# Optimization experiments

Measured on AMD Instinct MI355X. Metric: run time of the kernel, lower is better.

Reference implementation:

```python
import jax, jax.numpy as jnp
import numpy as np

N = 100000      # nodes
E = 1000000     # edges
G = 1024        # graphs
NODE_IN, CLIMBER_IN, HID, OUT, HEADS = 6, 4, 64, 4, 2
SLOPE = 0.2     # PyG GATConv default negative_slope


def gat_conv(x, edge_index, W, att_src, att_dst, bias):
    """PyG GATConv, heads=HEADS, concat=False (mean over heads), add_self_loops=True."""
    heads, ch = att_src.shape
    xp = (x @ W).reshape(-1, heads, ch)                       # [N,H,C]
    a_src = jnp.einsum('nhc,hc->nh', xp, att_src)             # [N,H]
    a_dst = jnp.einsum('nhc,hc->nh', xp, att_dst)
    loops = jnp.arange(x.shape[0])
    src = jnp.concatenate([edge_index[0], loops])             # [E+N]
    dst = jnp.concatenate([edge_index[1], loops])
    e = jax.nn.leaky_relu(a_src[src] + a_dst[dst], SLOPE)     # [E+N,H]
    emax = jax.ops.segment_max(e, dst, num_segments=x.shape[0])
    emax = jnp.where(jnp.isfinite(emax), emax, 0.0)
    ex = jnp.exp(e - emax[dst])
    den = jax.ops.segment_sum(ex, dst, num_segments=x.shape[0])
    alpha = ex / (den[dst] + 1e-16)                           # segment softmax over incoming edges
    msg = xp[src] * alpha[:, :, None]                         # [E+N,H,C]
    agg = jax.ops.segment_sum(msg, dst, num_segments=x.shape[0])  # [N,H,C]
    return agg.mean(axis=1) + bias                            # concat=False -> head mean


def setup_inputs() -> dict:
    key = jax.random.key(0)
    ks = jax.random.split(key, 20)
    s = lambda *d: 1.0 / np.sqrt(d[0])
    inp = {
        'x': jax.random.normal(ks[0], (N, NODE_IN), jnp.float32),
        'edge_index': jax.random.randint(ks[1], (2, E), 0, N),
        'batch': jnp.sort(jax.random.randint(ks[2], (N,), 0, G)),
        'climber': jax.random.normal(ks[3], (G, CLIMBER_IN), jnp.float32),
        # conv1 params
        'W1': jax.random.normal(ks[4], (NODE_IN, HEADS * HID), jnp.float32) * s(NODE_IN),
        'as1': jax.random.normal(ks[5], (HEADS, HID), jnp.float32) * s(HID),
        'ad1': jax.random.normal(ks[6], (HEADS, HID), jnp.float32) * s(HID),
        'b1': jnp.zeros((HID,), jnp.float32),
        # conv2 params
        'W2': jax.random.normal(ks[7], (HID, HEADS * HID), jnp.float32) * s(HID),
        'as2': jax.random.normal(ks[8], (HEADS, HID), jnp.float32) * s(HID),
        'ad2': jax.random.normal(ks[9], (HEADS, HID), jnp.float32) * s(HID),
        'b2': jnp.zeros((HID,), jnp.float32),
        # climber embed
        'Wc': jax.random.normal(ks[10], (CLIMBER_IN, HID), jnp.float32) * s(CLIMBER_IN),
        'bc': jnp.zeros((HID,), jnp.float32),
        # classifier
        'Wm1': jax.random.normal(ks[11], (2 * HID, HID), jnp.float32) * s(2 * HID),
        'bm1': jnp.zeros((HID,), jnp.float32),
        'Wm2': jax.random.normal(ks[12], (HID, OUT), jnp.float32) * s(HID),
        'bm2': jnp.zeros((OUT,), jnp.float32),
    }
    return inp


def reference(x, edge_index, batch, climber, W1, as1, ad1, b1, W2, as2, ad2, b2,
              Wc, bc, Wm1, bm1, Wm2, bm2):
    h = jax.nn.relu(gat_conv(x, edge_index, W1, as1, ad1, b1))
    h = jax.nn.relu(gat_conv(h, edge_index, W2, as2, ad2, b2))
    c = jax.nn.relu(climber @ Wc + bc)            # dropout is identity in eval mode
    z = jnp.concatenate([h, c[batch]], axis=1)    # [N, 2*HID]
    z = jax.nn.relu(z @ Wm1 + bm1)                # dropout identity (eval)
    return z @ Wm2 + bm2                          # [N, OUT]
```

## Files before the change

### kernel.cpp

```cpp
#include <hip/hip_runtime.h>
#include <hip/hip_fp16.h>

#define SLOPE 0.2f
#define BKW  512
#define BKSH 9
#define MAXB 256

typedef _Float16 half8 __attribute__((ext_vector_type(8)));
typedef float f32x4 __attribute__((ext_vector_type(4)));

__device__ __forceinline__ float lrelu(float v) { return v >= 0.f ? v : SLOPE * v; }

__device__ __forceinline__ unsigned pack2(float a, float b) {
    __half2 h = __floats2half2_rn(a, b);
    return *reinterpret_cast<unsigned*>(&h);
}
__device__ __forceinline__ float2 h2f(unsigned u) {
    __half2 h = *reinterpret_cast<__half2*>(&u);
    return __half22float2(h);
}

__device__ __forceinline__ void pk8(unsigned& A0, unsigned& A1, unsigned& A2, unsigned& A3,
                                    unsigned ap, uint4 u) {
    __half2 a = *reinterpret_cast<__half2*>(&ap);
    __half2* up = reinterpret_cast<__half2*>(&u);
    *reinterpret_cast<__half2*>(&A0) = __hfma2(up[0], a, *reinterpret_cast<__half2*>(&A0));
    *reinterpret_cast<__half2*>(&A1) = __hfma2(up[1], a, *reinterpret_cast<__half2*>(&A1));
    *reinterpret_cast<__half2*>(&A2) = __hfma2(up[2], a, *reinterpret_cast<__half2*>(&A2));
    *reinterpret_cast<__half2*>(&A3) = __hfma2(up[3], a, *reinterpret_cast<__half2*>(&A3));
}

__global__ __launch_bounds__(256)
void k_xp_gemm64h(const __half* __restrict__ x, const _Float16* __restrict__ W2t,
                  const float* __restrict__ as_, const float* __restrict__ ad_,
                  __half* __restrict__ xph, float* __restrict__ asrc,
                  float* __restrict__ adst, int N) {
    __shared__ __half lh[4][16][128];
    const int t = threadIdx.x;
    const int w = t >> 6, lane = t & 63;
    const int c8 = lane & 15, kgrp = lane >> 4;
    const int nr0 = blockIdx.x * 64 + w * 16;

    uint4 a0u = make_uint4(0u,0u,0u,0u), a1u = make_uint4(0u,0u,0u,0u);
    int ar = nr0 + c8;
    if (ar < N) {
        const uint4* hp = (const uint4*)(x + (size_t)ar * 64);
        a0u = hp[kgrp];
        a1u = hp[4 + kgrp];
    }
    half8 A0, A1;
    __builtin_memcpy(&A0, &a0u, 16);
    __builtin_memcpy(&A1, &a1u, 16);

    f32x4 acc[8];
    #pragma unroll
    for (int i = 0; i < 8; ++i) acc[i] = (f32x4){0.f, 0.f, 0.f, 0.f};

    #pragma unroll
    for (int ct = 0; ct < 8; ++ct) {
        const uint4* wp = (const uint4*)(W2t + (size_t)(ct * 16 + c8) * 64);
        uint4 b0u = wp[kgrp];
        uint4 b1u = wp[4 + kgrp];
        half8 B0, B1;
        __builtin_memcpy(&B0, &b0u, 16);
        __builtin_memcpy(&B1, &b1u, 16);
        acc[ct] = __builtin_amdgcn_mfma_f32_16x16x32_f16(A0, B0, acc[ct], 0, 0, 0);
        acc[ct] = __builtin_amdgcn_mfma_f32_16x16x32_f16(A1, B1, acc[ct], 0, 0, 0);
    }

    float ps0[4] = {0,0,0,0}, ps1[4] = {0,0,0,0};
    float pd0[4] = {0,0,0,0}, pd1[4] = {0,0,0,0};
    #pragma unroll
    for (int ct = 0; ct < 8; ++ct) {
        float av = as_[ct * 16 + c8];
        float dv = ad_[ct * 16 + c8];
        #pragma unroll
        for (int j = 0; j < 4; ++j) {
            float v = acc[ct][j];
            if (ct < 4) { ps0[j] += av * v; pd0[j] += dv * v; }
            else        { ps1[j] += av * v; pd1[j] += dv * v; }
        }
    }
    #pragma unroll
    for (int off = 1; off <= 8; off <<= 1) {
        #pragma unroll
        for (int j = 0; j < 4; ++j) {
            ps0[j] += __shfl_xor(ps0[j], off, 64);
            ps1[j] += __shfl_xor(ps1[j], off, 64);
            pd0[j] += __shfl_xor(pd0[j], off, 64);
            pd1[j] += __shfl_xor(pd1[j], off, 64);
        }
    }
    if (c8 == 0) {
        #pragma unroll
        for (int j = 0; j < 4; ++j) {
            int gn = nr0 + kgrp * 4 + j;
            if (gn < N) {
                asrc[gn * 2]     = ps0[j];
                asrc[gn * 2 + 1] = ps1[j];
                adst[gn * 2]     = pd0[j];
                adst[gn * 2 + 1] = pd1[j];
            }
        }
    }

    #pragma unroll
    for (int ct = 0; ct < 8; ++ct)
        #pragma unroll
        for (int j = 0; j < 4; ++j)
            lh[w][kgrp * 4 + j][ct * 16 + c8] = __float2half(acc[ct][j]);
    __syncthreads();
    {
        int r = lane >> 2, q = lane & 3;
        int gn = nr0 + r;
        if (gn < N) {
            const uint4* srow = (const uint4*)&lh[w][r][0];
            uint4* drow = (uint4*)(xph + (size_t)gn * 128);
            #pragma unroll
            for (int c4 = 0; c4 < 4; ++c4) drow[q * 4 + c4] = srow[q * 4 + c4];
        }
    }
}

__global__ __launch_bounds__(256)
void k_bcount(const int* __restrict__ dst, int* __restrict__ bkt_cnt, int E, int nb) {
    __shared__ int cnt[MAXB];
    int t = threadIdx.x;
    for (int i = t; i < MAXB; i += 256) cnt[i] = 0;
    __syncthreads();
    int be = blockIdx.x * 4096;
    int n = min(4096, E - be);
    const int4* d4 = (const int4*)(dst + be);
    #pragma unroll
    for (int i = 0; i < 4; ++i) {
        int j = t + 256 * i, r = j * 4;
        if (r < n) {
            int4 d = d4[j];
            if (r + 0 < n) atomicAdd(&cnt[d.x >> BKSH], 1);
            if (r + 1 < n) atomicAdd(&cnt[d.y >> BKSH], 1);
            if (r + 2 < n) atomicAdd(&cnt[d.z >> BKSH], 1);
            if (r + 3 < n) atomicAdd(&cnt[d.w >> BKSH], 1);
        }
    }
    __syncthreads();
    for (int b = t; b < nb; b += 256) if (cnt[b]) atomicAdd(&bkt_cnt[b], cnt[b]);
}

__global__ __launch_bounds__(256)
void k_bscan_prep(const int* __restrict__ bkt_cnt, int* __restrict__ bkt_base,
                  int* __restrict__ bkt_cur, int nb, int E,
                  const float* __restrict__ W2, _Float16* __restrict__ W2t) {
    int t = threadIdx.x;
    if (blockIdx.x == 1) {
        for (int i = t; i < 128 * 64; i += 256) {
            int c = i >> 6, k = i & 63;
            W2t[i] = (_Float16)W2[k * 128 + c];
        }
        return;
    }
    __shared__ int sh[256];
    int v = (t < nb) ? bkt_cnt[t] : 0;
    int orig = v;
    sh[t] = v; __syncthreads();
    for (int off = 1; off < 256; off <<= 1) {
        int u = (t >= off) ? sh[t - off] : 0;
        __syncthreads(); sh[t] += u; __syncthreads();
    }
    int base = sh[t] - orig;
    if (t < nb) { bkt_base[t] = base; bkt_cur[t] = base; }
    if (t == 0) bkt_base[nb] = E;
}

__global__ __launch_bounds__(256)
void k_part(const int* __restrict__ src, const int* __restrict__ dst,
            int* __restrict__ bkt_cur, unsigned* __restrict__ ebuf, int E) {
    __shared__ int cnt[MAXB];
    __shared__ int shift[MAXB];
    __shared__ int cur[MAXB];
    __shared__ int sh[256];
    __shared__ unsigned data[4096];
    __shared__ unsigned char bof[4096];
    int t = threadIdx.x;
    cnt[t] = 0;
    __syncthreads();
    int be = blockIdx.x * 4096;
    int n = min(4096, E - be);
    const int4* d4 = (const int4*)(dst + be);
    const int4* s4 = (const int4*)(src + be);
    #pragma unroll
    for (int i = 0; i < 4; ++i) {
        int j = t + 256 * i, r = j * 4;
        if (r < n) {
            int4 d = d4[j];
            if (r + 0 < n) atomicAdd(&cnt[d.x >> BKSH], 1);
            if (r + 1 < n) atomicAdd(&cnt[d.y >> BKSH], 1);
            if (r + 2 < n) atomicAdd(&cnt[d.z >> BKSH], 1);
            if (r + 3 < n) atomicAdd(&cnt[d.w >> BKSH], 1);
        }
    }
    __syncthreads();
    int v = cnt[t], orig = v;
    sh[t] = v; __syncthreads();
    for (int off = 1; off < 256; off <<= 1) {
        int u = (t >= off) ? sh[t - off] : 0;
        __syncthreads(); sh[t] += u; __syncthreads();
    }
    int lb = sh[t] - orig;
    cur[t] = lb;
    if (orig > 0) {
        int g = atomicAdd(&bkt_cur[t], orig);
        shift[t] = g - lb;
    }
    __syncthreads();
    #pragma unroll
    for (int i = 0; i < 4; ++i) {
        int j = t + 256 * i, r = j * 4;
        if (r < n) {
            int4 d = d4[j]; int4 s = s4[j];
            if (r + 0 < n) { int b = d.x >> BKSH; int p = atomicAdd(&cur[b], 1); data[p] = ((unsigned)s.x << BKSH) | (unsigned)(d.x & (BKW-1)); bof[p] = (unsigned char)b; }
            if (r + 1 < n) { int b = d.y >> BKSH; int p = atomicAdd(&cur[b], 1); data[p] = ((unsigned)s.y << BKSH) | (unsigned)(d.y & (BKW-1)); bof[p] = (unsigned char)b; }
            if (r + 2 < n) { int b = d.z >> BKSH; int p = atomicAdd(&cur[b], 1); data[p] = ((unsigned)s.z << BKSH) | (unsigned)(d.z & (BKW-1)); bof[p] = (unsigned char)b; }
            if (r + 3 < n) { int b = d.w >> BKSH; int p = atomicAdd(&cur[b], 1); data[p] = ((unsigned)s.w << BKSH) | (unsigned)(d.w & (BKW-1)); bof[p] = (unsigned char)b; }
        }
    }
    __syncthreads();
    for (int j = t; j < n; j += 256) {
        int b = bof[j];
        ebuf[shift[b] + j] = data[j];
    }
}

__global__ __launch_bounds__(256)
void k_build(const unsigned* __restrict__ ebuf, const int* __restrict__ bkt_base,
             int* __restrict__ rowptr, int* __restrict__ csr_src, int N, int E, int nb,
             const float* __restrict__ x, const float* __restrict__ W1,
             const float* __restrict__ as1, const float* __restrict__ ad1,
             __half* __restrict__ xph, float* __restrict__ asrc,
             float* __restrict__ adst,
             const float* __restrict__ climber, const float* __restrict__ Wc,
             const float* __restrict__ bc, const float* __restrict__ Wm1,
             const float* __restrict__ bm1, float* __restrict__ cpre, int G,
             int nTile) {
    __shared__ char smem[17408];
    __shared__ int sh[256];
    int bid = blockIdx.x;
    const int t = threadIdx.x;

    if (bid < nb) {
        int* deg = (int*)smem;
        int* pre = deg + 512;
        int* cur = pre + 512;
        int n0 = bid << BKSH;
        int nn = min(BKW, N - n0);
        int eb = bkt_base[bid], ee = bkt_base[bid + 1];
        for (int i = t; i < BKW; i += 256) deg[i] = 0;
        __syncthreads();
        for (int j = eb + t; j < ee; j += 256)
            atomicAdd(&deg[ebuf[j] & (BKW - 1)], 1);
        __syncthreads();
        int a = deg[2 * t], b2 = deg[2 * t + 1];
        int s = a + b2, orig = s;
        sh[t] = s; __syncthreads();
        for (int off = 1; off < 256; off <<= 1) {
            int u = (t >= off) ? sh[t - off] : 0;
            __syncthreads(); sh[t] += u; __syncthreads();
        }
        int base = sh[t] - orig;
        pre[2 * t] = base; pre[2 * t + 1] = base + a;
        cur[2 * t] = base; cur[2 * t + 1] = base + a;
        __syncthreads();
        for (int i = t; i < nn; i += 256) rowptr[n0 + i] = eb + pre[i];
        for (int j = eb + t; j < ee; j += 256) {
            unsigned e = ebuf[j];
            int lp = atomicAdd(&cur[e & (BKW - 1)], 1);
            csr_src[eb + lp] = (int)(e >> BKSH);
        }
        if (bid == 0 && t == 0) rowptr[N] = E;
        return;
    }
    bid -= nb;
    if (bid < nTile) {
        constexpr int K = 6, ZS = 7;
        float* smf = (float*)smem;
        float* zs = smf;
        float* ws = smf + 448;
        const int n0 = bid * 64;

        for (int i = t; i < K * 32; i += 256) ((float4*)ws)[i] = ((const float4*)W1)[i];
        for (int i = t; i < 64 * K; i += 256) {
            int n = i / K, k = i - n * K;
            int gn = n0 + n;
            zs[n * ZS + k] = (gn < N) ? x[(size_t)gn * K + k] : 0.f;
        }
        __syncthreads();

        const int tx = t & 15, ty = t >> 4;
        const int c0a = tx * 4;
        const int c0b = 64 + tx * 4;

        float4 asA = *(const float4*)(as1 + c0a);
        float4 asB = *(const float4*)(as1 + c0b);
        float4 adA = *(const float4*)(ad1 + c0a);
        float4 adB = *(const float4*)(ad1 + c0b);

        float acc[4][8];
        #pragma unroll
        for (int i = 0; i < 4; ++i)
            #pragma unroll
            for (int j = 0; j < 8; ++j) acc[i][j] = 0.f;

        for (int k = 0; k < K; ++k) {
            float4 w0 = *(const float4*)(ws + k * 128 + c0a);
            float4 w1 = *(const float4*)(ws + k * 128 + c0b);
            #pragma unroll
            for (int i = 0; i < 4; ++i) {
                float zv = zs[(ty * 4 + i) * ZS + k];
                acc[i][0] += zv * w0.x; acc[i][1] += zv * w0.y;
                acc[i][2] += zv * w0.z; acc[i][3] += zv * w0.w;
                acc[i][4] += zv * w1.x; acc[i][5] += zv * w1.y;
                acc[i][6] += zv * w1.z; acc[i][7] += zv * w1.w;
            }
        }

        #pragma unroll
        for (int i = 0; i < 4; ++i) {
            int nl = ty * 4 + i, gn = n0 + nl;
            if (gn < N) {
                uint2 ua, ub;
                ua.x = pack2(acc[i][0], acc[i][1]);
                ua.y = pack2(acc[i][2], acc[i][3]);
                ub.x = pack2(acc[i][4], acc[i][5]);
                ub.y = pack2(acc[i][6], acc[i][7]);
                *(uint2*)(xph + (size_t)gn * 128 + c0a) = ua;
                *(uint2*)(xph + (size_t)gn * 128 + c0b) = ub;
            }
            float ps0 = acc[i][0]*asA.x + acc[i][1]*asA.y + acc[i][2]*asA.z + acc[i][3]*asA.w;
            float ps1 = acc[i][4]*asB.x + acc[i][5]*asB.y + acc[i][6]*asB.z + acc[i][7]*asB.w;
            float pd0 = acc[i][0]*adA.x + acc[i][1]*adA.y + acc[i][2]*adA.z + acc[i][3]*adA.w;
            float pd1 = acc[i][4]*adB.x + acc[i][5]*adB.y + acc[i][6]*adB.z + acc[i][7]*adB.w;
            #pragma unroll
            for (int off = 1; off <= 8; off <<= 1) {
                ps0 += __shfl_xor(ps0, off, 64);
                ps1 += __shfl_xor(ps1, off, 64);
                pd0 += __shfl_xor(pd0, off, 64);
                pd1 += __shfl_xor(pd1, off, 64);
            }
            if (tx == 0 && gn < N) {
                asrc[gn * 2]     = ps0;
                asrc[gn * 2 + 1] = ps1;
                adst[gn * 2]     = pd0;
                adst[gn * 2 + 1] = pd1;
            }
        }
        return;
    }
    bid -= nTile;
    {
        float* smf = (float*)smem;
        float* ce   = smf;
        float* wm1b = smf + 256;
        for (int i = t; i < 1024; i += 256) ((float4*)wm1b)[i] = ((const float4*)Wm1)[1024 + i];
        int gl = t >> 6, c = t & 63;
        int g = bid * 4 + gl;
        float acc = bc[c];
        if (g < G)
            for (int k = 0; k < 4; ++k) acc += climber[g * 4 + k] * Wc[k * 64 + c];
        ce[gl * 64 + c] = fmaxf(acc, 0.f);
        __syncthreads();
        float o = bm1[c];
        for (int k = 0; k < 64; ++k) o += ce[gl * 64 + k] * wm1b[k * 64 + c];
        if (g < G) cpre[(size_t)g * 64 + c] = o;
    }
}

__global__ void k_ag(const int* __restrict__ rowptr, const int* __restrict__ csr_src,
                     const float* __restrict__ asrc, const float* __restrict__ adst,
                     const __half* __restrict__ xph, const float* __restrict__ b,
                     __half* __restrict__ hout, int N) {
    int tid = blockIdx.x * blockDim.x + threadIdx.x;
    int lane = threadIdx.x & 63;
    int wid = tid >> 6;
    int nw = (gridDim.x * blockDim.x) >> 6;
    const int l  = lane & 31;
    const int hh = lane >> 5;
    const int g4 = (lane >> 3) & 3;
    const int c8 = lane & 7;
    const int lofs = hh * 8 + c8;
    const uint4* xp4 = (const uint4*)xph;
    float4 bb0 = ((const float4*)b)[c8 * 2];
    float4 bb1 = ((const float4*)b)[c8 * 2 + 1];

    for (int n = wid; n < N; n += nw) {
        int rs = rowptr[n], re = rowptr[n + 1], cnt = re - rs;
        uint4 uself = xp4[(size_t)n * 16 + lofs];
        float a_dst = adst[n * 2 + hh];
        float eself = __expf(lrelu(asrc[n * 2 + hh] + a_dst));

        unsigned A0 = 0u, A1 = 0u, A2 = 0u, A3 = 0u;
        float den;

        if (cnt <= 32) {
            float ev = 0.f; int s_reg = n;
            if (l < cnt) {
                s_reg = csr_src[rs + l];
                ev = __expf(lrelu(asrc[s_reg * 2 + hh] + a_dst));
            }
            unsigned evp = pack2(ev, ev);
            if (g4 == 0) pk8(A0, A1, A2, A3, pack2(eself, eself), uself);

            const int base = (hh << 5) - rs;
            int e0 = rs;
            for (; e0 + 4 < re; e0 += 8) {
                int ea = e0 + g4, eb = e0 + 4 + g4;
                unsigned aa = __shfl(evp,   base + ea, 64);
                int      sa = __shfl(s_reg, base + ea, 64);
                unsigned ab = __shfl(evp,   base + eb, 64);
                int      sb = __shfl(s_reg, base + eb, 64);
                if (eb >= re) { ab = 0u; sb = n; }
                uint4 u1 = xp4[(size_t)sa * 16 + lofs];
                uint4 u2 = xp4[(size_t)sb * 16 + lofs];
                pk8(A0, A1, A2, A3, aa, u1);
                pk8(A0, A1, A2, A3, ab, u2);
            }
            if (e0 < re) {
                int ea = e0 + g4;
                unsigned aa = __shfl(evp,   base + ea, 64);
                int      sa = __shfl(s_reg, base + ea, 64);
                if (ea >= re) { aa = 0u; sa = n; }
                uint4 u1 = xp4[(size_t)sa * 16 + lofs];
                pk8(A0, A1, A2, A3, aa, u1);
            }
            den = ev + (l == 0 ? eself : 0.f);
            #pragma unroll
            for (int off = 16; off > 0; off >>= 1) den += __shfl_xor(den, off, 64);
        } else {
            den = (l == 0) ? eself : 0.f;
            for (int e = rs + l; e < re; e += 32)
                den += __expf(lrelu(asrc[csr_src[e] * 2 + hh] + a_dst));
            #pragma unroll
            for (int off = 16; off > 0; off >>= 1) den += __shfl_xor(den, off, 64);
            if (g4 == 0) pk8(A0, A1, A2, A3, pack2(eself, eself), uself);
            for (int e0 = rs; e0 < re; e0 += 8) {
                int ea = e0 + g4, eb = e0 + 4 + g4;
                bool va = ea < re, vb = eb < re;
                int sa = va ? csr_src[ea] : n;
                int sb = vb ? csr_src[eb] : n;
                float fa = va ? __expf(lrelu(asrc[sa * 2 + hh] + a_dst)) : 0.f;
                float fb = vb ? __expf(lrelu(asrc[sb * 2 + hh] + a_dst)) : 0.f;
                unsigned aa = pack2(fa, fa);
                unsigned ab = pack2(fb, fb);
                uint4 u1 = xp4[(size_t)sa * 16 + lofs];
                uint4 u2 = xp4[(size_t)sb * 16 + lofs];
                pk8(A0, A1, A2, A3, aa, u1);
                pk8(A0, A1, A2, A3, ab, u2);
            }
        }

        float inv = 1.f / (den + 1e-16f);

        float2 f0 = h2f(A0), f1 = h2f(A1), f2 = h2f(A2), f3 = h2f(A3);
        float4 accA = make_float4(f0.x, f0.y, f1.x, f1.y);
        float4 accB = make_float4(f2.x, f2.y, f3.x, f3.y);

        #pragma unroll
        for (int off = 8; off <= 16; off <<= 1) {
            accA.x += __shfl_xor(accA.x, off, 64);
            accA.y += __shfl_xor(accA.y, off, 64);
            accA.z += __shfl_xor(accA.z, off, 64);
            accA.w += __shfl_xor(accA.w, off, 64);
            accB.x += __shfl_xor(accB.x, off, 64);
            accB.y += __shfl_xor(accB.y, off, 64);
            accB.z += __shfl_xor(accB.z, off, 64);
            accB.w += __shfl_xor(accB.w, off, 64);
        }
        accA.x *= inv; accA.y *= inv; accA.z *= inv; accA.w *= inv;
        accB.x *= inv; accB.y *= inv; accB.z *= inv; accB.w *= inv;
        accA.x += __shfl_xor(accA.x, 32, 64);
        accA.y += __shfl_xor(accA.y, 32, 64);
        accA.z += __shfl_xor(accA.z, 32, 64);
        accA.w += __shfl_xor(accA.w, 32, 64);
        accB.x += __shfl_xor(accB.x, 32, 64);
        accB.y += __shfl_xor(accB.y, 32, 64);
        accB.z += __shfl_xor(accB.z, 32, 64);
        accB.w += __shfl_xor(accB.w, 32, 64);

        if (lane < 8) {
            uint4 up;
            up.x = pack2(fmaxf(accA.x * 0.5f + bb0.x, 0.f),
                         fmaxf(accA.y * 0.5f + bb0.y, 0.f));
            up.y = pack2(fmaxf(accA.z * 0.5f + bb0.z, 0.f),
                         fmaxf(accA.w * 0.5f + bb0.w, 0.f));
            up.z = pack2(fmaxf(accB.x * 0.5f + bb1.x, 0.f),
                         fmaxf(accB.y * 0.5f + bb1.y, 0.f));
            up.w = pack2(fmaxf(accB.z * 0.5f + bb1.z, 0.f),
                         fmaxf(accB.w * 0.5f + bb1.w, 0.f));
            ((uint4*)hout)[(size_t)n * 8 + c8] = up;
        }
    }
}

__global__ __launch_bounds__(256)
void k_final(const __half* __restrict__ h2, const float* __restrict__ cpre,
             const int* __restrict__ batch, const float* __restrict__ Wm1,
             const float* __restrict__ Wm2, const float* __restrict__ bm2,
             float* __restrict__ out, int N) {
    __shared__ float zs[64 * 65];
    __shared__ float ws[64 * 64];
    __shared__ float4 w2l[64];
    const int n0 = blockIdx.x * 64;
    const int t = threadIdx.x;

    for (int i = t; i < 1024; i += 256) ((float4*)ws)[i] = ((const float4*)Wm1)[i];
    if (t < 64) w2l[t] = ((const float4*)Wm2)[t];
    for (int i = t; i < 64 * 8; i += 256) {
        int n = i >> 3, k8 = i & 7;
        int gn = n0 + n;
        uint4 v = make_uint4(0u, 0u, 0u, 0u);
        if (gn < N) v = ((const uint4*)h2)[(size_t)gn * 8 + k8];
        float2 f0 = h2f(v.x), f1 = h2f(v.y), f2 = h2f(v.z), f3 = h2f(v.w);
        float* zr = zs + n * 65 + k8 * 8;
        zr[0] = f0.x; zr[1] = f0.y; zr[2] = f1.x; zr[3] = f1.y;
        zr[4] = f2.x; zr[5] = f2.y; zr[6] = f3.x; zr[7] = f3.y;
    }
    __syncthreads();

    const int tx = t & 15, ty = t >> 4;
    const int c0 = tx * 4;
    float acc[4][4];
    #pragma unroll
    for (int i = 0; i < 4; ++i)
        #pragma unroll
        for (int j = 0; j < 4; ++j) acc[i][j] = 0.f;

    for (int k = 0; k < 64; ++k) {
        float4 wv = *(const float4*)(ws + k * 64 + c0);
        #pragma unroll
        for (int i = 0; i < 4; ++i) {
            float zv = zs[(ty * 4 + i) * 65 + k];
            acc[i][0] += zv * wv.x; acc[i][1] += zv * wv.y;
            acc[i][2] += zv * wv.z; acc[i][3] += zv * wv.w;
        }
    }
    __syncthreads();

    float4 wa = w2l[c0], wb = w2l[c0 + 1], wc = w2l[c0 + 2], wd = w2l[c0 + 3];
    #pragma unroll
    for (int i = 0; i < 4; ++i) {
        int nl = ty * 4 + i, gn = n0 + nl;
        float4 o = make_float4(0.f, 0.f, 0.f, 0.f);
        if (gn < N) {
            int b = batch[gn];
            float4 cp = *(const float4*)(cpre + (size_t)b * 64 + c0);
            float m0 = fmaxf(acc[i][0] + cp.x, 0.f);
            float m1 = fmaxf(acc[i][1] + cp.y, 0.f);
            float m2 = fmaxf(acc[i][2] + cp.z, 0.f);
            float m3 = fmaxf(acc[i][3] + cp.w, 0.f);
            o.x = m0 * wa.x + m1 * wb.x + m2 * wc.x + m3 * wd.x;
            o.y = m0 * wa.y + m1 * wb.y + m2 * wc.y + m3 * wd.y;
            o.z = m0 * wa.z + m1 * wb.z + m2 * wc.z + m3 * wd.z;
            o.w = m0 * wa.w + m1 * wb.w + m2 * wc.w + m3 * wd.w;
        }
        *(float4*)(zs + tx * 260 + nl * 4) = o;
    }
    __syncthreads();
    {
        int nl = t >> 2, j = t & 3, gn = n0 + nl;
        float s = 0.f;
        #pragma unroll
        for (int tx2 = 0; tx2 < 16; ++tx2) s += zs[tx2 * 260 + nl * 4 + j];
        if (gn < N) out[(size_t)gn * 4 + j] = s + bm2[j];
    }
}

extern "C" void kernel_launch(void* const* d_in, const int* in_sizes, int n_in,
                              void* d_out, int out_size, void* d_ws, size_t ws_size,
                              hipStream_t stream) {
    const float* x       = (const float*)d_in[0];
    const int*   ei      = (const int*)  d_in[1];
    const int*   batch   = (const int*)  d_in[2];
    const float* climber = (const float*)d_in[3];
    const float* W1  = (const float*)d_in[4];
    const float* as1 = (const float*)d_in[5];
    const float* ad1 = (const float*)d_in[6];
    const float* b1  = (const float*)d_in[7];
    const float* W2  = (const float*)d_in[8];
    const float* as2 = (const float*)d_in[9];
    const float* ad2 = (const float*)d_in[10];
    const float* b2  = (const float*)d_in[11];
    const float* Wc  = (const float*)d_in[12];
    const float* bc  = (const float*)d_in[13];
    const float* Wm1 = (const float*)d_in[14];
    const float* bm1 = (const float*)d_in[15];
    const float* Wm2 = (const float*)d_in[16];
    const float* bm2 = (const float*)d_in[17];

    const int N  = in_sizes[0] / 6;
    const int E  = in_sizes[1] / 2;
    const int G  = in_sizes[3] / 4;

    const int* srcI = ei;
    const int* dstI = ei + E;

    char* base = (char*)d_ws;
    size_t off = 0;
    auto carve = [&](size_t bytes) { void* p = base + off; off += (bytes + 255) & ~size_t(255); return p; };
    __half* xph    = (__half*)carve((size_t)N * 128 * 2);
    __half* hbuf   = (__half*)carve((size_t)N * 64 * 2);
    float* asrc    = (float*)carve((size_t)N * 2 * 4);
    float* adst    = (float*)carve((size_t)N * 2 * 4);
    float* cpre    = (float*)carve((size_t)G * 64 * 4);
    int*   rowptr  = (int*)  carve((size_t)(N + 1) * 4);
    int*   csr_src = (int*)  carve((size_t)E * 4);
    unsigned* ebuf = (unsigned*)carve((size_t)E * 4);
    int*   bkt_cnt = (int*)  carve((size_t)MAXB * 4);
    int*   bkt_base= (int*)  carve((size_t)(MAXB + 1) * 4);
    int*   bkt_cur = (int*)  carve((size_t)MAXB * 4);
    _Float16* W2t  = (_Float16*)carve((size_t)128 * 64 * 2);

    const int tpb = 256;
    const int nb = (N + BKW - 1) >> BKSH;
    const int nChunk = (E + 4095) / 4096;
    const int nClimber = (G + 3) / 4;
    const int PG = 2048;
    const int nTile = (N + 63) / 64;

    hipMemsetAsync(bkt_cnt, 0, (size_t)nb * 4, stream);
    k_bcount<<<nChunk, tpb, 0, stream>>>(dstI, bkt_cnt, E, nb);
    k_bscan_prep<<<2, tpb, 0, stream>>>(bkt_cnt, bkt_base, bkt_cur, nb, E, W2, W2t);
    k_part<<<nChunk, tpb, 0, stream>>>(srcI, dstI, bkt_cur, ebuf, E);
    k_build<<<nb + nTile + nClimber, tpb, 0, stream>>>(
        ebuf, bkt_base, rowptr, csr_src, N, E, nb,
        x, W1, as1, ad1, xph, asrc, adst,
        climber, Wc, bc, Wm1, bm1, cpre, G, nTile);

    k_ag<<<PG, tpb, 0, stream>>>(rowptr, csr_src, asrc, adst, xph, b1, hbuf, N);

    k_xp_gemm64h<<<nTile, tpb, 0, stream>>>(hbuf, W2t, as2, ad2, xph, asrc, adst, N);
    k_ag<<<PG, tpb, 0, stream>>>(rowptr, csr_src, asrc, adst, xph, b2, hbuf, N);

    k_final<<<nTile, tpb, 0, stream>>>(hbuf, cpre, batch, Wm1, Wm2, bm2, (float*)d_out, N);
}
```

Baseline: 276.6 us.

## Use MFMA for final classifier GEMM and replace bucket-count atomics with partials

The final classifier kernel now computes the 64x64 hidden-layer matmul with fp16 MFMA instructions, reading the hidden features directly into registers. It uses a pre-transposed fp16 copy of Wm1 and reduces the output projection with wave shuffles instead of fp32 FMA loops through shared memory. Separately, bucket counting writes per-block partial histograms that the scan kernel sums, removing the global atomics and the memset launch. The costs are lower-precision arithmetic in the classifier and a serial sum over about 245 chunks in the scan block.

```diff
diff --git a/kernel.cpp b/kernel.cpp
--- a/kernel.cpp
+++ b/kernel.cpp
@@ -123,7 +123,7 @@
 }
 
 __global__ __launch_bounds__(256)
-void k_bcount(const int* __restrict__ dst, int* __restrict__ bkt_cnt, int E, int nb) {
+void k_bcount(const int* __restrict__ dst, int* __restrict__ partial, int E) {
     __shared__ int cnt[MAXB];
     int t = threadIdx.x;
     for (int i = t; i < MAXB; i += 256) cnt[i] = 0;
@@ -143,13 +143,15 @@
         }
     }
     __syncthreads();
-    for (int b = t; b < nb; b += 256) if (cnt[b]) atomicAdd(&bkt_cnt[b], cnt[b]);
+    int* outp = partial + blockIdx.x * MAXB;
+    for (int b = t; b < MAXB; b += 256) outp[b] = cnt[b];
 }
 
 __global__ __launch_bounds__(256)
-void k_bscan_prep(const int* __restrict__ bkt_cnt, int* __restrict__ bkt_base,
-                  int* __restrict__ bkt_cur, int nb, int E,
-                  const float* __restrict__ W2, _Float16* __restrict__ W2t) {
+void k_bscan_prep(const int* __restrict__ partial, int* __restrict__ bkt_base,
+                  int* __restrict__ bkt_cur, int nb, int E, int nChunk,
+                  const float* __restrict__ W2, _Float16* __restrict__ W2t,
+                  const float* __restrict__ Wm1, _Float16* __restrict__ Wm1t) {
     int t = threadIdx.x;
     if (blockIdx.x == 1) {
         for (int i = t; i < 128 * 64; i += 256) {
@@ -158,8 +160,17 @@
         }
         return;
     }
+    if (blockIdx.x == 2) {
+        for (int i = t; i < 64 * 64; i += 256) {
+            int c = i >> 6, k = i & 63;
+            Wm1t[i] = (_Float16)Wm1[k * 64 + c];
+        }
+        return;
+    }
     __shared__ int sh[256];
-    int v = (t < nb) ? bkt_cnt[t] : 0;
+    int s = 0;
+    for (int c = 0; c < nChunk; ++c) s += partial[c * MAXB + t];
+    int v = (t < nb) ? s : 0;
     int orig = v;
     sh[t] = v; __syncthreads();
     for (int off = 1; off < 256; off <<= 1) {
@@ -501,74 +512,87 @@
 
 __global__ __launch_bounds__(256)
 void k_final(const __half* __restrict__ h2, const float* __restrict__ cpre,
-             const int* __restrict__ batch, const float* __restrict__ Wm1,
+             const int* __restrict__ batch, const _Float16* __restrict__ Wm1t,
              const float* __restrict__ Wm2, const float* __restrict__ bm2,
              float* __restrict__ out, int N) {
-    __shared__ float zs[64 * 65];
-    __shared__ float ws[64 * 64];
     __shared__ float4 w2l[64];
-    const int n0 = blockIdx.x * 64;
     const int t = threadIdx.x;
-
-    for (int i = t; i < 1024; i += 256) ((float4*)ws)[i] = ((const float4*)Wm1)[i];
+    const int w = t >> 6, lane = t & 63;
+    const int c8 = lane & 15, kgrp = lane >> 4;
+    const int nr0 = blockIdx.x * 64 + w * 16;
+
     if (t < 64) w2l[t] = ((const float4*)Wm2)[t];
-    for (int i = t; i < 64 * 8; i += 256) {
-        int n = i >> 3, k8 = i & 7;
-        int gn = n0 + n;
-        uint4 v = make_uint4(0u, 0u, 0u, 0u);
-        if (gn < N) v = ((const uint4*)h2)[(size_t)gn * 8 + k8];
-        float2 f0 = h2f(v.x), f1 = h2f(v.y), f2 = h2f(v.z), f3 = h2f(v.w);
-        float* zr = zs + n * 65 + k8 * 8;
-        zr[0] = f0.x; zr[1] = f0.y; zr[2] = f1.x; zr[3] = f1.y;
-        zr[4] = f2.x; zr[5] = f2.y; zr[6] = f3.x; zr[7] = f3.y;
-    }
-    __syncthreads();
-
-    const int tx = t & 15, ty = t >> 4;
-    const int c0 = tx * 4;
-    float acc[4][4];
-    #pragma unroll
-    for (int i = 0; i < 4; ++i)
-        #pragma unroll
-        for (int j = 0; j < 4; ++j) acc[i][j] = 0.f;
-
-    for (int k = 0; k < 64; ++k) {
-        float4 wv = *(const float4*)(ws + k * 64 + c0);
-        #pragma unroll
-        for (int i = 0; i < 4; ++i) {
-            float zv = zs[(ty * 4 + i) * 65 + k];
-            acc[i][0] += zv * wv.x; acc[i][1] += zv * wv.y;
-            acc[i][2] += zv * wv.z; acc[i][3] += zv * wv.w;
-        }
-    }
-    __syncthreads();
-
-    float4 wa = w2l[c0], wb = w2l[c0 + 1], wc = w2l[c0 + 2], wd = w2l[c0 + 3];
-    #pragma unroll
-    for (int i = 0; i < 4; ++i) {
-        int nl = ty * 4 + i, gn = n0 + nl;
-        float4 o = make_float4(0.f, 0.f, 0.f, 0.f);
-        if (gn < N) {
-            int b = batch[gn];
-            float4 cp = *(const float4*)(cpre + (size_t)b * 64 + c0);
-            float m0 = fmaxf(acc[i][0] + cp.x, 0.f);
-            float m1 = fmaxf(acc[i][1] + cp.y, 0.f);
-            float m2 = fmaxf(acc[i][2] + cp.z, 0.f);
-            float m3 = fmaxf(acc[i][3] + cp.w, 0.f);
-            o.x = m0 * wa.x + m1 * wb.x + m2 * wc.x + m3 * wd.x;
-            o.y = m0 * wa.y + m1 * wb.y + m2 * wc.y + m3 * wd.y;
-            o.z = m0 * wa.z + m1 * wb.z + m2 * wc.z + m3 * wd.z;
-            o.w = m0 * wa.w + m1 * wb.w + m2 * wc.w + m3 * wd.w;
-        }
-        *(float4*)(zs + tx * 260 + nl * 4) = o;
-    }
-    __syncthreads();
-    {
-        int nl = t >> 2, j = t & 3, gn = n0 + nl;
-        float s = 0.f;
-        #pragma unroll
-        for (int tx2 = 0; tx2 < 16; ++tx2) s += zs[tx2 * 260 + nl * 4 + j];
-        if (gn < N) out[(size_t)gn * 4 + j] = s + bm2[j];
+
+    uint4 a0u = make_uint4(0u,0u,0u,0u), a1u = make_uint4(0u,0u,0u,0u);
+    int ar = nr0 + c8;
+    if (ar < N) {
+        const uint4* hp = (const uint4*)(h2 + (size_t)ar * 64);
+        a0u = hp[kgrp];
+        a1u = hp[4 + kgrp];
+    }
+    half8 A0, A1;
+    __builtin_memcpy(&A0, &a0u, 16);
+    __builtin_memcpy(&A1, &a1u, 16);
+
+    f32x4 acc[4];
+    #pragma unroll
+    for (int i = 0; i < 4; ++i) acc[i] = (f32x4){0.f, 0.f, 0.f, 0.f};
+    __syncthreads();
+
+    #pragma unroll
+    for (int ct = 0; ct < 4; ++ct) {
+        const uint4* wp = (const uint4*)(Wm1t + (size_t)(ct * 16 + c8) * 64);
+        uint4 b0u = wp[kgrp];
+        uint4 b1u = wp[4 + kgrp];
+        half8 B0, B1;
+        __builtin_memcpy(&B0, &b0u, 16);
+        __builtin_memcpy(&B1, &b1u, 16);
+        acc[ct] = __builtin_amdgcn_mfma_f32_16x16x32_f16(A0, B0, acc[ct], 0, 0, 0);
+        acc[ct] = __builtin_amdgcn_mfma_f32_16x16x32_f16(A1, B1, acc[ct], 0, 0, 0);
+    }
+
+    int bidx[4];
+    #pragma unroll
+    for (int j = 0; j < 4; ++j) {
+        int gn = nr0 + kgrp * 4 + j;
+        bidx[j] = (gn < N) ? batch[gn] : 0;
+    }
+    float4 o[4];
+    #pragma unroll
+    for (int j = 0; j < 4; ++j) o[j] = make_float4(0.f, 0.f, 0.f, 0.f);
+    #pragma unroll
+    for (int ct = 0; ct < 4; ++ct) {
+        float4 wv = w2l[ct * 16 + c8];
+        #pragma unroll
+        for (int j = 0; j < 4; ++j) {
+            float cp = cpre[(size_t)bidx[j] * 64 + ct * 16 + c8];
+            float m = fmaxf(acc[ct][j] + cp, 0.f);
+            o[j].x += m * wv.x; o[j].y += m * wv.y;
+            o[j].z += m * wv.z; o[j].w += m * wv.w;
+        }
+    }
+    #pragma unroll
+    for (int off = 1; off <= 8; off <<= 1) {
+        #pragma unroll
+        for (int j = 0; j < 4; ++j) {
+            o[j].x += __shfl_xor(o[j].x, off, 64);
+            o[j].y += __shfl_xor(o[j].y, off, 64);
+            o[j].z += __shfl_xor(o[j].z, off, 64);
+            o[j].w += __shfl_xor(o[j].w, off, 64);
+        }
+    }
+    if (c8 == 0) {
+        float4 bmv = *(const float4*)bm2;
+        #pragma unroll
+        for (int j = 0; j < 4; ++j) {
+            int gn = nr0 + kgrp * 4 + j;
+            if (gn < N) {
+                float4 r;
+                r.x = o[j].x + bmv.x; r.y = o[j].y + bmv.y;
+                r.z = o[j].z + bmv.z; r.w = o[j].w + bmv.w;
+                ((float4*)out)[gn] = r;
+            }
+        }
     }
 }
 
@@ -612,21 +636,22 @@
     int*   rowptr  = (int*)  carve((size_t)(N + 1) * 4);
     int*   csr_src = (int*)  carve((size_t)E * 4);
     unsigned* ebuf = (unsigned*)carve((size_t)E * 4);
-    int*   bkt_cnt = (int*)  carve((size_t)MAXB * 4);
     int*   bkt_base= (int*)  carve((size_t)(MAXB + 1) * 4);
     int*   bkt_cur = (int*)  carve((size_t)MAXB * 4);
     _Float16* W2t  = (_Float16*)carve((size_t)128 * 64 * 2);
+    _Float16* Wm1t = (_Float16*)carve((size_t)64 * 64 * 2);
 
     const int tpb = 256;
     const int nb = (N + BKW - 1) >> BKSH;
     const int nChunk = (E + 4095) / 4096;
+    int* partial = (int*)carve((size_t)nChunk * MAXB * 4);
     const int nClimber = (G + 3) / 4;
     const int PG = 2048;
     const int nTile = (N + 63) / 64;
 
-    hipMemsetAsync(bkt_cnt, 0, (size_t)nb * 4, stream);
-    k_bcount<<<nChunk, tpb, 0, stream>>>(dstI, bkt_cnt, E, nb);
-    k_bscan_prep<<<2, tpb, 0, stream>>>(bkt_cnt, bkt_base, bkt_cur, nb, E, W2, W2t);
+    k_bcount<<<nChunk, tpb, 0, stream>>>(dstI, partial, E);
+    k_bscan_prep<<<3, tpb, 0, stream>>>(partial, bkt_base, bkt_cur, nb, E, nChunk,
+                                        W2, W2t, Wm1, Wm1t);
     k_part<<<nChunk, tpb, 0, stream>>>(srcI, dstI, bkt_cur, ebuf, E);
     k_build<<<nb + nTile + nClimber, tpb, 0, stream>>>(
         ebuf, bkt_base, rowptr, csr_src, N, E, nb,
@@ -638,5 +663,5 @@
     k_xp_gemm64h<<<nTile, tpb, 0, stream>>>(hbuf, W2t, as2, ad2, xph, asrc, adst, N);
     k_ag<<<PG, tpb, 0, stream>>>(rowptr, csr_src, asrc, adst, xph, b2, hbuf, N);
 
-    k_final<<<nTile, tpb, 0, stream>>>(hbuf, cpre, batch, Wm1, Wm2, bm2, (float*)d_out, N);
-}
+    k_final<<<nTile, tpb, 0, stream>>>(hbuf, cpre, batch, Wm1t, Wm2, bm2, (float*)d_out, N);
+}
```

After: 294.6 us. 1.07x slower.
